# Kernel optimization log

Measured on AMD Instinct MI355X. Metric: run time of the kernel, lower is better.

The kernel has to match this reference:

```python
import jax, jax.numpy as jnp
import numpy as np

BLOCK_SPLIT = (4, 4, 4)
GRID = 256
N_BLOCK = 64
BX = GRID // 4  # 64, per-block grid resolution along each axis
N_PTS = 4_194_304


def setup_inputs() -> dict:
    key = jax.random.key(0)
    k1, k2 = jax.random.split(key)
    aabb = jnp.array([[-1.5, -1.5, -1.5], [1.5, 1.5, 1.5]], dtype=jnp.float32)
    # points roughly inside the aabb
    xyz_sampled = jax.random.uniform(k1, (N_PTS, 3), dtype=jnp.float32) * 3.0 - 1.5
    alpha_volume = jax.random.uniform(k2, (GRID, GRID, GRID), dtype=jnp.float32)
    # per-block domains (as kilonerf global_to_local expects): block AABBs
    idx = np.stack(np.meshgrid(np.arange(4), np.arange(4), np.arange(4), indexing='ij'), -1).reshape(-1, 3)
    voxel = np.array([3.0 / 4.0] * 3)
    dmin = (-1.5 + idx * voxel).astype(np.float32)
    dmax = (dmin + voxel).astype(np.float32)
    return {"xyz_sampled": xyz_sampled, "aabb": aabb, "alpha_volume": alpha_volume,
            "domain_min": jnp.asarray(dmin), "domain_max": jnp.asarray(dmax)}


def _sample_alpha(xyz, aabb, alpha_volume, dmin, dmax):
    bs = jnp.asarray(BLOCK_SPLIT, jnp.float32)
    voxel = (aabb[1] - aabb[0]) / bs                      # per-block world size
    idx3 = jnp.floor((xyz - aabb[0]) / voxel).astype(jnp.int32)
    idx3 = jnp.clip(idx3, 0, jnp.array(BLOCK_SPLIT, jnp.int32) - 1)  # edge clamp (matches loop)
    strides = jnp.array([BLOCK_SPLIT[2] * BLOCK_SPLIT[1], BLOCK_SPLIT[2], 1], jnp.int32)
    bid = (idx3 * strides).sum(-1)                        # [N] block id in [0, 64)

    order = jnp.argsort(bid)                              # jax sort is stable; matches bucket-by-block order
    bid_s = bid[order]
    pts = xyz[order]

    # global_to_local (kilonerf): map into per-block [-1,1]^3
    local = 2.0 * (pts - dmin[bid_s]) / (dmax[bid_s] - dmin[bid_s]) - 1.0  # [N,3] (gx,gy,gz)

    # torch .view(64,1,64,64,64) is a raw contiguous reinterpretation -> plain reshape
    vols = alpha_volume.reshape(N_BLOCK, BX, BX, BX)      # [B, D, H, W]
    D = H = W = BX
    # grid_sample convention: grid x -> W axis, y -> H axis, z -> D axis; align_corners=True
    fx = (local[:, 0] + 1.0) * 0.5 * (W - 1)
    fy = (local[:, 1] + 1.0) * 0.5 * (H - 1)
    fz = (local[:, 2] + 1.0) * 0.5 * (D - 1)
    x0 = jnp.floor(fx); y0 = jnp.floor(fy); z0 = jnp.floor(fz)
    wx = fx - x0; wy = fy - y0; wz = fz - z0
    x0i = x0.astype(jnp.int32); y0i = y0.astype(jnp.int32); z0i = z0.astype(jnp.int32)

    def fetch(zi, yi, xi):
        # zeros padding for out-of-range corners (grid_sample padding_mode='zeros')
        inb = (zi >= 0) & (zi < D) & (yi >= 0) & (yi < H) & (xi >= 0) & (xi < W)
        v = vols[bid_s, jnp.clip(zi, 0, D - 1), jnp.clip(yi, 0, H - 1), jnp.clip(xi, 0, W - 1)]
        return jnp.where(inb, v, 0.0)

    out = jnp.zeros_like(fx)
    for dz, wz_ in ((0, 1.0 - wz), (1, wz)):
        for dy, wy_ in ((0, 1.0 - wy), (1, wy)):
            for dx, wx_ in ((0, 1.0 - wx), (1, wx)):
                out = out + wz_ * wy_ * wx_ * fetch(z0i + dz, y0i + dy, x0i + dx)
    return out  # [N] alpha values in block-sorted order


def reference(xyz_sampled, aabb, alpha_volume, domain_min, domain_max):
    return _sample_alpha(xyz_sampled, aabb, alpha_volume, domain_min, domain_max)
```

## Files before the change

### kernel.cpp

```cpp
#include <hip/hip_runtime.h>

#define TILE  4096
#define BLK   256
#define NBUCK 64

__device__ __forceinline__ int compute_bid(float px, float py, float pz,
                                           float a0x, float a0y, float a0z,
                                           float vx, float vy, float vz) {
    int ix = (int)floorf((px - a0x) / vx);
    int iy = (int)floorf((py - a0y) / vy);
    int iz = (int)floorf((pz - a0z) / vz);
    ix = min(max(ix, 0), 3);
    iy = min(max(iy, 0), 3);
    iz = min(max(iz, 0), 3);
    return ix * 16 + iy * 4 + iz;
}

__global__ void hist_kernel(const float* __restrict__ xyz,
                            const float* __restrict__ aabb,
                            int* __restrict__ hist, int N, int G) {
    __shared__ int s_h[NBUCK];
    const int tid = threadIdx.x, g = blockIdx.x;
    if (tid < NBUCK) s_h[tid] = 0;
    __syncthreads();
    const float a0x = aabb[0], a0y = aabb[1], a0z = aabb[2];
    const float vx = (aabb[3] - a0x) * 0.25f;
    const float vy = (aabb[4] - a0y) * 0.25f;
    const float vz = (aabb[5] - a0z) * 0.25f;
    for (int c = 0; c < TILE / (BLK * 4); ++c) {
        int p0 = g * TILE + c * (BLK * 4) + tid * 4;
        if (p0 + 3 < N) {
            const float4* v4 = (const float4*)(xyz + (size_t)p0 * 3);
            float4 f0 = v4[0], f1 = v4[1], f2 = v4[2];
            int b0 = compute_bid(f0.x, f0.y, f0.z, a0x, a0y, a0z, vx, vy, vz);
            int b1 = compute_bid(f0.w, f1.x, f1.y, a0x, a0y, a0z, vx, vy, vz);
            int b2 = compute_bid(f1.z, f1.w, f2.x, a0x, a0y, a0z, vx, vy, vz);
            int b3 = compute_bid(f2.y, f2.z, f2.w, a0x, a0y, a0z, vx, vy, vz);
            atomicAdd(&s_h[b0], 1);
            atomicAdd(&s_h[b1], 1);
            atomicAdd(&s_h[b2], 1);
            atomicAdd(&s_h[b3], 1);
        } else {
            for (int k = 0; k < 4; ++k) {
                int i = p0 + k;
                if (i < N) {
                    int b = compute_bid(xyz[3 * i], xyz[3 * i + 1], xyz[3 * i + 2],
                                        a0x, a0y, a0z, vx, vy, vz);
                    atomicAdd(&s_h[b], 1);
                }
            }
        }
    }
    __syncthreads();
    if (tid < NBUCK) hist[tid * G + g] = s_h[tid];
}

__global__ void scan_rows_kernel(int* __restrict__ hist, int* __restrict__ tot, int G) {
    __shared__ int sh[BLK];
    const int b = blockIdx.x, t = threadIdx.x;
    const int L = (G + BLK - 1) / BLK;
    const int lo = t * L;
    const int n = min(L, max(0, G - lo));
    const int base = b * G + lo;
    int s = 0;
    for (int k = 0; k < n; ++k) s += hist[base + k];
    sh[t] = s;
    __syncthreads();
    for (int off = 1; off < BLK; off <<= 1) {
        int v = (t >= off) ? sh[t - off] : 0;
        __syncthreads();
        sh[t] += v;
        __syncthreads();
    }
    int excl = (t == 0) ? 0 : sh[t - 1];
    for (int k = 0; k < n; ++k) {
        int v = hist[base + k];
        hist[base + k] = excl;
        excl += v;
    }
    if (t == BLK - 1) tot[b] = sh[BLK - 1];
}

__global__ void scan_buckets_kernel(const int* __restrict__ tot, int* __restrict__ off) {
    __shared__ int sh[NBUCK];
    const int t = threadIdx.x;
    sh[t] = tot[t];
    __syncthreads();
    for (int o = 1; o < NBUCK; o <<= 1) {
        int v = (t >= o) ? sh[t - o] : 0;
        __syncthreads();
        sh[t] += v;
        __syncthreads();
    }
    off[t] = (t == 0) ? 0 : sh[t - 1];
}

__global__ void scatter_payload_kernel(const float* __restrict__ xyz,
                                       const float* __restrict__ aabb,
                                       const float* __restrict__ dmin,
                                       const float* __restrict__ dmax,
                                       const int* __restrict__ hist,
                                       const int* __restrict__ off,
                                       float4* __restrict__ payload, int N, int G) {
    __shared__ int   s_cnt[NBUCK];
    __shared__ int   s_whist[4][NBUCK];
    __shared__ float s_dmin[192], s_dmax[192];
    const int tid = threadIdx.x, g = blockIdx.x;
    if (tid < NBUCK) s_cnt[tid] = hist[tid * G + g] + off[tid];
    for (int i = tid; i < 192; i += BLK) {
        s_dmin[i] = dmin[i];
        s_dmax[i] = dmax[i];
    }
    const float a0x = aabb[0], a0y = aabb[1], a0z = aabb[2];
    const float vx = (aabb[3] - a0x) * 0.25f;
    const float vy = (aabb[4] - a0y) * 0.25f;
    const float vz = (aabb[5] - a0z) * 0.25f;
    __syncthreads();

    const int lane = tid & 63;
    const int wv = tid >> 6;
    const unsigned long long lt = (1ull << lane) - 1ull;

    for (int c = 0; c < TILE / BLK; ++c) {
        int i = g * TILE + c * BLK + tid;
        bool valid = (i < N);
        int b = 0;
        float fx = 0.0f, fy = 0.0f, fz = 0.0f;
        if (valid) {
            float px = xyz[3 * i], py = xyz[3 * i + 1], pz = xyz[3 * i + 2];
            b = compute_bid(px, py, pz, a0x, a0y, a0z, vx, vy, vz);
            float dn0 = s_dmin[3 * b], dn1 = s_dmin[3 * b + 1], dn2 = s_dmin[3 * b + 2];
            float dM0 = s_dmax[3 * b], dM1 = s_dmax[3 * b + 1], dM2 = s_dmax[3 * b + 2];
            float lx = 2.0f * (px - dn0) / (dM0 - dn0) - 1.0f;
            float ly = 2.0f * (py - dn1) / (dM1 - dn1) - 1.0f;
            float lz = 2.0f * (pz - dn2) / (dM2 - dn2) - 1.0f;
            fx = (lx + 1.0f) * 0.5f * 63.0f;
            fy = (ly + 1.0f) * 0.5f * 63.0f;
            fz = (lz + 1.0f) * 0.5f * 63.0f;
        }
        ((int*)s_whist)[tid] = 0;
        __syncthreads();
        unsigned long long m = __ballot(valid);
        #pragma unroll
        for (int k = 0; k < 6; ++k) {
            unsigned long long bal = __ballot((b >> k) & 1);
            m &= ((b >> k) & 1) ? bal : ~bal;
        }
        int rank = __popcll(m & lt);
        if (valid && rank == 0) s_whist[wv][b] = __popcll(m);
        __syncthreads();
        if (valid) {
            int pos = s_cnt[b] + rank;
            for (int w2 = 0; w2 < wv; ++w2) pos += s_whist[w2][b];
            payload[pos] = make_float4(fx, fy, fz, __int_as_float(b));
        }
        __syncthreads();
        if (tid < NBUCK)
            s_cnt[tid] += s_whist[0][tid] + s_whist[1][tid] +
                          s_whist[2][tid] + s_whist[3][tid];
        __syncthreads();
    }
}

__global__ void gather_out_kernel(const float* __restrict__ vol,
                                  const float4* __restrict__ payload,
                                  float* __restrict__ out, int N) {
    int nb = gridDim.x;
    int d = blockIdx.x;
    int lb = (nb % 8 == 0) ? (d % 8) * (nb / 8) + (d / 8) : d;
    int j = lb * BLK + threadIdx.x;
    if (j >= N) return;
    float4 p = payload[j];
    float fx = p.x, fy = p.y, fz = p.z;
    int b = __float_as_int(p.w);
    float x0f = floorf(fx), y0f = floorf(fy), z0f = floorf(fz);
    float wx = fx - x0f, wy = fy - y0f, wz = fz - z0f;
    int x0 = (int)x0f, y0 = (int)y0f, z0 = (int)z0f;
    const float* vb = vol + ((size_t)b << 18);
    auto F = [&](int zi, int yi, int xi) -> float {
        if ((unsigned)zi >= 64u || (unsigned)yi >= 64u || (unsigned)xi >= 64u)
            return 0.0f;
        return vb[(zi << 12) + (yi << 6) + xi];
    };
    float s = 0.0f;
    s += (1.0f - wz) * (1.0f - wy) * (1.0f - wx) * F(z0,     y0,     x0);
    s += (1.0f - wz) * (1.0f - wy) * wx          * F(z0,     y0,     x0 + 1);
    s += (1.0f - wz) * wy          * (1.0f - wx) * F(z0,     y0 + 1, x0);
    s += (1.0f - wz) * wy          * wx          * F(z0,     y0 + 1, x0 + 1);
    s += wz          * (1.0f - wy) * (1.0f - wx) * F(z0 + 1, y0,     x0);
    s += wz          * (1.0f - wy) * wx          * F(z0 + 1, y0,     x0 + 1);
    s += wz          * wy          * (1.0f - wx) * F(z0 + 1, y0 + 1, x0);
    s += wz          * wy          * wx          * F(z0 + 1, y0 + 1, x0 + 1);
    out[j] = s;
}

extern "C" void kernel_launch(void* const* d_in, const int* in_sizes, int n_in,
                              void* d_out, int out_size, void* d_ws, size_t ws_size,
                              hipStream_t stream) {
    const float* xyz  = (const float*)d_in[0];
    const float* aabb = (const float*)d_in[1];
    const float* vol  = (const float*)d_in[2];
    const float* dmin = (const float*)d_in[3];
    const float* dmax = (const float*)d_in[4];
    float* out = (float*)d_out;
    const int N = in_sizes[0] / 3;
    const int G = (N + TILE - 1) / TILE;

    char* ws = (char*)d_ws;
    float4* payload = (float4*)ws;
    int* hist = (int*)(ws + (size_t)N * 16);
    int* tot  = (int*)(ws + (size_t)N * 16 + (size_t)NBUCK * G * 4);
    int* off  = (int*)(ws + (size_t)N * 16 + (size_t)NBUCK * G * 4 + 256);

    hist_kernel<<<G, BLK, 0, stream>>>(xyz, aabb, hist, N, G);
    scan_rows_kernel<<<NBUCK, BLK, 0, stream>>>(hist, tot, G);
    scan_buckets_kernel<<<1, NBUCK, 0, stream>>>(tot, off);
    scatter_payload_kernel<<<G, BLK, 0, stream>>>(xyz, aabb, dmin, dmax, hist, off,
                                                  payload, N, G);
    gather_out_kernel<<<(N + BLK - 1) / BLK, BLK, 0, stream>>>(vol, payload, out, N);
}
```

Baseline: 292.0 us.

## Bin points into 4096 sub-block cells and gather from LDS-staged volume tiles

Points are keyed by block and 16^3 sub-cell, with a second histogram and scan over 4096 cells. The scatter writes each payload into its cell's contiguous range via a global atomic and records the original output index. The gather then runs one workgroup per cell, staging a 17^3 volume tile in shared memory, and scatters results back to block-sorted output positions. This targets the random global volume reads in the gather, at the cost of extra kernels, a keys buffer, contended global atomics and scattered output writes.

```diff
diff --git a/kernel.cpp b/kernel.cpp
--- a/kernel.cpp
+++ b/kernel.cpp
@@ -1,8 +1,9 @@
 #include <hip/hip_runtime.h>
 
-#define TILE  4096
 #define BLK   256
-#define NBUCK 64
+#define TILE  8192
+#define NB    64
+#define NF    4096
 
 __device__ __forceinline__ int compute_bid(float px, float py, float pz,
                                            float a0x, float a0y, float a0z,
@@ -16,48 +17,83 @@
     return ix * 16 + iy * 4 + iz;
 }
 
+__device__ __forceinline__ int compute_key(float px, float py, float pz,
+                                           float a0x, float a0y, float a0z,
+                                           float vx, float vy, float vz,
+                                           const float* s_dn, const float* s_sc,
+                                           int& b, float& fx, float& fy, float& fz) {
+    b = compute_bid(px, py, pz, a0x, a0y, a0z, vx, vy, vz);
+    fx = (px - s_dn[3 * b])     * s_sc[3 * b];
+    fy = (py - s_dn[3 * b + 1]) * s_sc[3 * b + 1];
+    fz = (pz - s_dn[3 * b + 2]) * s_sc[3 * b + 2];
+    int icx = min(max((int)floorf(fx) >> 4, 0), 3);
+    int icy = min(max((int)floorf(fy) >> 4, 0), 3);
+    int icz = min(max((int)floorf(fz) >> 4, 0), 3);
+    return (b << 6) | (icz << 4) | (icy << 2) | icx;
+}
+
 __global__ void hist_kernel(const float* __restrict__ xyz,
                             const float* __restrict__ aabb,
-                            int* __restrict__ hist, int N, int G) {
-    __shared__ int s_h[NBUCK];
+                            const float* __restrict__ dmin,
+                            const float* __restrict__ dmax,
+                            int* __restrict__ hist64,
+                            unsigned short* __restrict__ keys, int N, int G) {
+    __shared__ int   sh[NF];
+    __shared__ float s_dn[192], s_sc[192];
     const int tid = threadIdx.x, g = blockIdx.x;
-    if (tid < NBUCK) s_h[tid] = 0;
-    __syncthreads();
+    for (int l = tid; l < NF; l += BLK) sh[l] = 0;
+    for (int l = tid; l < 192; l += BLK) {
+        s_dn[l] = dmin[l];
+        s_sc[l] = 63.0f / (dmax[l] - dmin[l]);
+    }
     const float a0x = aabb[0], a0y = aabb[1], a0z = aabb[2];
     const float vx = (aabb[3] - a0x) * 0.25f;
     const float vy = (aabb[4] - a0y) * 0.25f;
     const float vz = (aabb[5] - a0z) * 0.25f;
+    __syncthreads();
     for (int c = 0; c < TILE / (BLK * 4); ++c) {
         int p0 = g * TILE + c * (BLK * 4) + tid * 4;
         if (p0 + 3 < N) {
             const float4* v4 = (const float4*)(xyz + (size_t)p0 * 3);
             float4 f0 = v4[0], f1 = v4[1], f2 = v4[2];
-            int b0 = compute_bid(f0.x, f0.y, f0.z, a0x, a0y, a0z, vx, vy, vz);
-            int b1 = compute_bid(f0.w, f1.x, f1.y, a0x, a0y, a0z, vx, vy, vz);
-            int b2 = compute_bid(f1.z, f1.w, f2.x, a0x, a0y, a0z, vx, vy, vz);
-            int b3 = compute_bid(f2.y, f2.z, f2.w, a0x, a0y, a0z, vx, vy, vz);
-            atomicAdd(&s_h[b0], 1);
-            atomicAdd(&s_h[b1], 1);
-            atomicAdd(&s_h[b2], 1);
-            atomicAdd(&s_h[b3], 1);
+            int b; float fx, fy, fz;
+            int k0 = compute_key(f0.x, f0.y, f0.z, a0x, a0y, a0z, vx, vy, vz, s_dn, s_sc, b, fx, fy, fz);
+            int k1 = compute_key(f0.w, f1.x, f1.y, a0x, a0y, a0z, vx, vy, vz, s_dn, s_sc, b, fx, fy, fz);
+            int k2 = compute_key(f1.z, f1.w, f2.x, a0x, a0y, a0z, vx, vy, vz, s_dn, s_sc, b, fx, fy, fz);
+            int k3 = compute_key(f2.y, f2.z, f2.w, a0x, a0y, a0z, vx, vy, vz, s_dn, s_sc, b, fx, fy, fz);
+            atomicAdd(&sh[k0], 1); atomicAdd(&sh[k1], 1);
+            atomicAdd(&sh[k2], 1); atomicAdd(&sh[k3], 1);
+            keys[p0]     = (unsigned short)k0;
+            keys[p0 + 1] = (unsigned short)k1;
+            keys[p0 + 2] = (unsigned short)k2;
+            keys[p0 + 3] = (unsigned short)k3;
         } else {
-            for (int k = 0; k < 4; ++k) {
-                int i = p0 + k;
+            for (int t = 0; t < 4; ++t) {
+                int i = p0 + t;
                 if (i < N) {
-                    int b = compute_bid(xyz[3 * i], xyz[3 * i + 1], xyz[3 * i + 2],
-                                        a0x, a0y, a0z, vx, vy, vz);
-                    atomicAdd(&s_h[b], 1);
+                    int b; float fx, fy, fz;
+                    int k = compute_key(xyz[3 * i], xyz[3 * i + 1], xyz[3 * i + 2],
+                                        a0x, a0y, a0z, vx, vy, vz, s_dn, s_sc, b, fx, fy, fz);
+                    atomicAdd(&sh[k], 1);
+                    keys[i] = (unsigned short)k;
                 }
             }
         }
     }
     __syncthreads();
-    if (tid < NBUCK) hist[tid * G + g] = s_h[tid];
-}
-
-__global__ void scan_rows_kernel(int* __restrict__ hist, int* __restrict__ tot, int G) {
+    if (tid < NB) {
+        int s = 0;
+        #pragma unroll
+        for (int j = 0; j < 64; ++j) s += sh[tid * 64 + j];
+        hist64[tid * G + g] = s;
+    }
+}
+
+__global__ void scan_rows_kernel(int* __restrict__ hist, int* __restrict__ tot,
+                                 int* __restrict__ tot4096, int G) {
     __shared__ int sh[BLK];
     const int b = blockIdx.x, t = threadIdx.x;
+    if (b == 0) for (int l = t; l < NF; l += BLK) tot4096[l] = 0;
     const int L = (G + BLK - 1) / BLK;
     const int lo = t * L;
     const int n = min(L, max(0, G - lo));
@@ -81,12 +117,27 @@
     if (t == BLK - 1) tot[b] = sh[BLK - 1];
 }
 
+__global__ void fhist_kernel(const unsigned short* __restrict__ keys,
+                             int* __restrict__ tot4096, int N) {
+    __shared__ int sh[NF];
+    const int tid = threadIdx.x;
+    for (int l = tid; l < NF; l += BLK) sh[l] = 0;
+    __syncthreads();
+    const int per = (N + gridDim.x - 1) / gridDim.x;
+    const int lo = blockIdx.x * per;
+    const int hi = min(lo + per, N);
+    for (int i = lo + tid; i < hi; i += BLK) atomicAdd(&sh[keys[i]], 1);
+    __syncthreads();
+    for (int l = tid; l < NF; l += BLK)
+        if (sh[l]) atomicAdd(&tot4096[l], sh[l]);
+}
+
 __global__ void scan_buckets_kernel(const int* __restrict__ tot, int* __restrict__ off) {
-    __shared__ int sh[NBUCK];
+    __shared__ int sh[NB];
     const int t = threadIdx.x;
     sh[t] = tot[t];
     __syncthreads();
-    for (int o = 1; o < NBUCK; o <<= 1) {
+    for (int o = 1; o < NB; o <<= 1) {
         int v = (t >= o) ? sh[t - o] : 0;
         __syncthreads();
         sh[t] += v;
@@ -95,26 +146,50 @@
     off[t] = (t == 0) ? 0 : sh[t - 1];
 }
 
-__global__ void scatter_payload_kernel(const float* __restrict__ xyz,
-                                       const float* __restrict__ aabb,
-                                       const float* __restrict__ dmin,
-                                       const float* __restrict__ dmax,
-                                       const int* __restrict__ hist,
-                                       const int* __restrict__ off,
-                                       float4* __restrict__ payload, int N, int G) {
-    __shared__ int   s_cnt[NBUCK];
-    __shared__ int   s_whist[4][NBUCK];
-    __shared__ float s_dmin[192], s_dmax[192];
+__global__ void fscan_kernel(const int* __restrict__ tot4096,
+                             int* __restrict__ foff, int* __restrict__ fcnt) {
+    __shared__ int sh[BLK];
+    const int t = threadIdx.x;
+    const int L = NF / BLK;
+    int loc[16];
+    int s = 0;
+    #pragma unroll
+    for (int j = 0; j < L; ++j) { loc[j] = tot4096[t * L + j]; s += loc[j]; }
+    sh[t] = s;
+    __syncthreads();
+    for (int o = 1; o < BLK; o <<= 1) {
+        int v = (t >= o) ? sh[t - o] : 0;
+        __syncthreads();
+        sh[t] += v;
+        __syncthreads();
+    }
+    int run = (t == 0) ? 0 : sh[t - 1];
+    #pragma unroll
+    for (int j = 0; j < L; ++j) {
+        foff[t * L + j] = run;
+        fcnt[t * L + j] = run;
+        run += loc[j];
+    }
+    if (t == BLK - 1) foff[NF] = run;
+}
+
+__global__ void scatter_kernel(const float* __restrict__ xyz,
+                               const float* __restrict__ dmin,
+                               const float* __restrict__ dmax,
+                               const unsigned short* __restrict__ keys,
+                               const int* __restrict__ hist64,
+                               const int* __restrict__ off64,
+                               int* __restrict__ fcnt,
+                               float4* __restrict__ payload, int N, int G) {
+    __shared__ int   s_cnt[NB];
+    __shared__ int   s_whist[4][NB];
+    __shared__ float s_dn[192], s_sc[192];
     const int tid = threadIdx.x, g = blockIdx.x;
-    if (tid < NBUCK) s_cnt[tid] = hist[tid * G + g] + off[tid];
-    for (int i = tid; i < 192; i += BLK) {
-        s_dmin[i] = dmin[i];
-        s_dmax[i] = dmax[i];
-    }
-    const float a0x = aabb[0], a0y = aabb[1], a0z = aabb[2];
-    const float vx = (aabb[3] - a0x) * 0.25f;
-    const float vy = (aabb[4] - a0y) * 0.25f;
-    const float vz = (aabb[5] - a0z) * 0.25f;
+    if (tid < NB) s_cnt[tid] = hist64[tid * G + g] + off64[tid];
+    for (int l = tid; l < 192; l += BLK) {
+        s_dn[l] = dmin[l];
+        s_sc[l] = 63.0f / (dmax[l] - dmin[l]);
+    }
     __syncthreads();
 
     const int lane = tid & 63;
@@ -124,74 +199,84 @@
     for (int c = 0; c < TILE / BLK; ++c) {
         int i = g * TILE + c * BLK + tid;
         bool valid = (i < N);
-        int b = 0;
+        int k = 0, b = 0;
         float fx = 0.0f, fy = 0.0f, fz = 0.0f;
         if (valid) {
+            k = keys[i];
+            b = k >> 6;
             float px = xyz[3 * i], py = xyz[3 * i + 1], pz = xyz[3 * i + 2];
-            b = compute_bid(px, py, pz, a0x, a0y, a0z, vx, vy, vz);
-            float dn0 = s_dmin[3 * b], dn1 = s_dmin[3 * b + 1], dn2 = s_dmin[3 * b + 2];
-            float dM0 = s_dmax[3 * b], dM1 = s_dmax[3 * b + 1], dM2 = s_dmax[3 * b + 2];
-            float lx = 2.0f * (px - dn0) / (dM0 - dn0) - 1.0f;
-            float ly = 2.0f * (py - dn1) / (dM1 - dn1) - 1.0f;
-            float lz = 2.0f * (pz - dn2) / (dM2 - dn2) - 1.0f;
-            fx = (lx + 1.0f) * 0.5f * 63.0f;
-            fy = (ly + 1.0f) * 0.5f * 63.0f;
-            fz = (lz + 1.0f) * 0.5f * 63.0f;
+            fx = (px - s_dn[3 * b])     * s_sc[3 * b];
+            fy = (py - s_dn[3 * b + 1]) * s_sc[3 * b + 1];
+            fz = (pz - s_dn[3 * b + 2]) * s_sc[3 * b + 2];
         }
         ((int*)s_whist)[tid] = 0;
         __syncthreads();
         unsigned long long m = __ballot(valid);
         #pragma unroll
-        for (int k = 0; k < 6; ++k) {
-            unsigned long long bal = __ballot((b >> k) & 1);
-            m &= ((b >> k) & 1) ? bal : ~bal;
+        for (int q = 0; q < 6; ++q) {
+            unsigned long long bal = __ballot((b >> q) & 1);
+            m &= ((b >> q) & 1) ? bal : ~bal;
         }
         int rank = __popcll(m & lt);
         if (valid && rank == 0) s_whist[wv][b] = __popcll(m);
         __syncthreads();
         if (valid) {
-            int pos = s_cnt[b] + rank;
-            for (int w2 = 0; w2 < wv; ++w2) pos += s_whist[w2][b];
-            payload[pos] = make_float4(fx, fy, fz, __int_as_float(b));
+            int outpos = s_cnt[b] + rank;
+            for (int w2 = 0; w2 < wv; ++w2) outpos += s_whist[w2][b];
+            int fpos = atomicAdd(&fcnt[k], 1);
+            payload[fpos] = make_float4(fx, fy, fz, __int_as_float(outpos));
         }
         __syncthreads();
-        if (tid < NBUCK)
+        if (tid < NB)
             s_cnt[tid] += s_whist[0][tid] + s_whist[1][tid] +
                           s_whist[2][tid] + s_whist[3][tid];
         __syncthreads();
     }
 }
 
-__global__ void gather_out_kernel(const float* __restrict__ vol,
-                                  const float4* __restrict__ payload,
-                                  float* __restrict__ out, int N) {
-    int nb = gridDim.x;
-    int d = blockIdx.x;
-    int lb = (nb % 8 == 0) ? (d % 8) * (nb / 8) + (d / 8) : d;
-    int j = lb * BLK + threadIdx.x;
-    if (j >= N) return;
-    float4 p = payload[j];
-    float fx = p.x, fy = p.y, fz = p.z;
-    int b = __float_as_int(p.w);
-    float x0f = floorf(fx), y0f = floorf(fy), z0f = floorf(fz);
-    float wx = fx - x0f, wy = fy - y0f, wz = fz - z0f;
-    int x0 = (int)x0f, y0 = (int)y0f, z0 = (int)z0f;
+__global__ void __launch_bounds__(BLK) gather_kernel(
+        const float* __restrict__ vol,
+        const float4* __restrict__ payload,
+        const int* __restrict__ foff,
+        float* __restrict__ out) {
+    __shared__ float sv[17 * 17 * 17];
+    const int tid = threadIdx.x, k = blockIdx.x;
+    const int b = k >> 6;
+    const int bz = ((k >> 4) & 3) * 16, by = ((k >> 2) & 3) * 16, bx = (k & 3) * 16;
     const float* vb = vol + ((size_t)b << 18);
-    auto F = [&](int zi, int yi, int xi) -> float {
-        if ((unsigned)zi >= 64u || (unsigned)yi >= 64u || (unsigned)xi >= 64u)
-            return 0.0f;
-        return vb[(zi << 12) + (yi << 6) + xi];
-    };
-    float s = 0.0f;
-    s += (1.0f - wz) * (1.0f - wy) * (1.0f - wx) * F(z0,     y0,     x0);
-    s += (1.0f - wz) * (1.0f - wy) * wx          * F(z0,     y0,     x0 + 1);
-    s += (1.0f - wz) * wy          * (1.0f - wx) * F(z0,     y0 + 1, x0);
-    s += (1.0f - wz) * wy          * wx          * F(z0,     y0 + 1, x0 + 1);
-    s += wz          * (1.0f - wy) * (1.0f - wx) * F(z0 + 1, y0,     x0);
-    s += wz          * (1.0f - wy) * wx          * F(z0 + 1, y0,     x0 + 1);
-    s += wz          * wy          * (1.0f - wx) * F(z0 + 1, y0 + 1, x0);
-    s += wz          * wy          * wx          * F(z0 + 1, y0 + 1, x0 + 1);
-    out[j] = s;
+    for (int l = tid; l < 17 * 17 * 17; l += BLK) {
+        int z = l / 289, r = l - z * 289, y = r / 17, x = r - y * 17;
+        int gz = bz + z, gy = by + y, gx = bx + x;
+        sv[l] = (gz < 64 && gy < 64 && gx < 64)
+                    ? vb[(gz << 12) + (gy << 6) + gx] : 0.0f;
+    }
+    __syncthreads();
+    const int lo = foff[k];
+    const int n = foff[k + 1] - lo;
+    for (int j = tid; j < n; j += BLK) {
+        float4 p = payload[lo + j];
+        float x0f = floorf(p.x), y0f = floorf(p.y), z0f = floorf(p.z);
+        float wx = p.x - x0f, wy = p.y - y0f, wz = p.z - z0f;
+        int x0 = (int)x0f, y0 = (int)y0f, z0 = (int)z0f;
+        auto F = [&](int gz, int gy, int gx) -> float {
+            if ((unsigned)gz >= 64u || (unsigned)gy >= 64u || (unsigned)gx >= 64u)
+                return 0.0f;
+            int lz = gz - bz, ly = gy - by, lx = gx - bx;
+            if ((unsigned)lz <= 16u && (unsigned)ly <= 16u && (unsigned)lx <= 16u)
+                return sv[lz * 289 + ly * 17 + lx];
+            return vb[(gz << 12) + (gy << 6) + gx];
+        };
+        float s = 0.0f;
+        s += (1.0f - wz) * (1.0f - wy) * (1.0f - wx) * F(z0,     y0,     x0);
+        s += (1.0f - wz) * (1.0f - wy) * wx          * F(z0,     y0,     x0 + 1);
+        s += (1.0f - wz) * wy          * (1.0f - wx) * F(z0,     y0 + 1, x0);
+        s += (1.0f - wz) * wy          * wx          * F(z0,     y0 + 1, x0 + 1);
+        s += wz          * (1.0f - wy) * (1.0f - wx) * F(z0 + 1, y0,     x0);
+        s += wz          * (1.0f - wy) * wx          * F(z0 + 1, y0,     x0 + 1);
+        s += wz          * wy          * (1.0f - wx) * F(z0 + 1, y0 + 1, x0);
+        s += wz          * wy          * wx          * F(z0 + 1, y0 + 1, x0 + 1);
+        out[__float_as_int(p.w)] = s;
+    }
 }
 
 extern "C" void kernel_launch(void* const* d_in, const int* in_sizes, int n_in,
@@ -207,15 +292,22 @@
     const int G = (N + TILE - 1) / TILE;
 
     char* ws = (char*)d_ws;
-    float4* payload = (float4*)ws;
-    int* hist = (int*)(ws + (size_t)N * 16);
-    int* tot  = (int*)(ws + (size_t)N * 16 + (size_t)NBUCK * G * 4);
-    int* off  = (int*)(ws + (size_t)N * 16 + (size_t)NBUCK * G * 4 + 256);
-
-    hist_kernel<<<G, BLK, 0, stream>>>(xyz, aabb, hist, N, G);
-    scan_rows_kernel<<<NBUCK, BLK, 0, stream>>>(hist, tot, G);
-    scan_buckets_kernel<<<1, NBUCK, 0, stream>>>(tot, off);
-    scatter_payload_kernel<<<G, BLK, 0, stream>>>(xyz, aabb, dmin, dmax, hist, off,
-                                                  payload, N, G);
-    gather_out_kernel<<<(N + BLK - 1) / BLK, BLK, 0, stream>>>(vol, payload, out, N);
-}
+    size_t o = 0;
+    float4* payload = (float4*)(ws + o);          o += (size_t)N * 16;
+    unsigned short* keys = (unsigned short*)(ws + o); o += ((size_t)N * 2 + 255) & ~255ull;
+    int* hist64  = (int*)(ws + o);                o += ((size_t)NB * G * 4 + 255) & ~255ull;
+    int* tot64   = (int*)(ws + o);                o += 256;
+    int* off64   = (int*)(ws + o);                o += 256;
+    int* tot4096 = (int*)(ws + o);                o += (size_t)NF * 4;
+    int* foff    = (int*)(ws + o);                o += ((size_t)(NF + 1) * 4 + 255) & ~255ull;
+    int* fcnt    = (int*)(ws + o);                o += (size_t)NF * 4;
+
+    hist_kernel<<<G, BLK, 0, stream>>>(xyz, aabb, dmin, dmax, hist64, keys, N, G);
+    scan_rows_kernel<<<NB, BLK, 0, stream>>>(hist64, tot64, tot4096, G);
+    fhist_kernel<<<128, BLK, 0, stream>>>(keys, tot4096, N);
+    scan_buckets_kernel<<<1, NB, 0, stream>>>(tot64, off64);
+    fscan_kernel<<<1, BLK, 0, stream>>>(tot4096, foff, fcnt);
+    scatter_kernel<<<G, BLK, 0, stream>>>(xyz, dmin, dmax, keys, hist64, off64,
+                                          fcnt, payload, N, G);
+    gather_kernel<<<NF, BLK, 0, stream>>>(vol, payload, foff, out);
+}
```

After: 535.6 us. 1.83x slower.
